# Kernel tuning notes

Measured on AMD Instinct MI355X. Metric: run time of the kernel, lower is better.

Reference implementation:

```python
import jax, jax.numpy as jnp
import numpy as np

N_NODES = 50000
N_EDGES = 800000
C_IN = 64
C_HID = 64


def setup_inputs() -> dict:
    key = jax.random.key(0)
    k1, k2, k3, k4, k5 = jax.random.split(key, 5)
    x = jax.random.normal(k1, (N_NODES, C_IN), dtype=jnp.float32)
    edge_index = jax.random.randint(k2, (2, N_EDGES), 0, N_NODES, dtype=jnp.int64)
    edge_attr = jax.random.uniform(k3, (N_EDGES, 1), dtype=jnp.float32)
    # SplineConv params: kernel weight (K=1 collapsed), root weight, bias
    W = jax.random.normal(k4, (C_IN, C_HID), dtype=jnp.float32) * (1.0 / np.sqrt(C_IN))
    root = jax.random.normal(k5, (C_IN, C_HID), dtype=jnp.float32) * (1.0 / np.sqrt(C_IN))
    bias = jnp.zeros((C_HID,), dtype=jnp.float32)
    return {"x": x, "edge_index": edge_index, "edge_attr": edge_attr,
            "W": W, "root": root, "bias": bias}


def reference(x, edge_index, edge_attr, W, root, bias):
    # SplineConv(dim=1, kernel_size=1): the B-spline basis weights sum to 1
    # over the single kernel, so message_j = x_j @ W exactly (edge_attr drops out).
    src = edge_index[0]  # source nodes j
    dst = edge_index[1]  # target nodes i
    n = x.shape[0]
    h = x @ W                                   # [N, H] transform once per node
    msg_sum = jax.ops.segment_sum(h[src], dst, num_segments=n)   # scatter-add [N, H]
    deg = jax.ops.segment_sum(jnp.ones_like(dst, dtype=h.dtype), dst, num_segments=n)
    agg = msg_sum / jnp.clip(deg, 1.0)[:, None]  # mean aggregation
    out = agg + x @ root + bias                  # root weight + bias
    return jax.nn.relu(out)
```

## Files before the change

### kernel.cpp

```cpp
#include <hip/hip_runtime.h>

#define N_NODES 50000
#define N_EDGES 800000
#define C 64
#define BUCKET_NODES 256
#define NBUCK 196
#define BUCKET_CAP 6144
#define BIN_CHUNK 4096
#define NBIN_BLOCKS 196
#define PREP_XBLOCKS 315
#define PB_BLOCKS (1 + PREP_XBLOCKS + NBIN_BLOCKS)
#define BIN0 (1 + PREP_XBLOCKS)
#define AGG_NODES 16
#define NAGG (N_NODES / AGG_NODES)
#define LDSTR 72

typedef __attribute__((ext_vector_type(8))) short bf16x8;
typedef __attribute__((ext_vector_type(4))) float f32x4;

__device__ inline unsigned short f2bf(float f) {
    union { float f; unsigned u; } v; v.f = f;
    unsigned r = v.u + 0x7FFF + ((v.u >> 16) & 1);
    return (unsigned short)(r >> 16);
}
__device__ inline float bf2f(unsigned short h) {
    union { unsigned u; float f; } v; v.u = (unsigned)h << 16;
    return v.f;
}

__global__ __launch_bounds__(256) void zero_cursor(int* __restrict__ c)
{
    c[threadIdx.x] = 0;
}

__global__ __launch_bounds__(256) void prep_bin(
    const float* __restrict__ x,
    const float* __restrict__ W,
    const float* __restrict__ R,
    const int*   __restrict__ ei,
    unsigned short* __restrict__ xbf,
    unsigned* __restrict__ xf8w,
    uint4* __restrict__ wpack,
    int* __restrict__ bucketCursor,
    int* __restrict__ bucketbuf)
{
    const int bid = blockIdx.x;

    if (bid == 0) {
        for (int s = threadIdx.x; s < 1024; s += 256) {
            const int f    = s >> 6;
            const int lane = s & 63;
            const int mat  = f >> 3, ks = (f >> 2) & 1, ct = f & 3;
            const float* src = mat ? R : W;
            const int kbase = ks * 32 + (lane >> 4) * 8;
            const int col   = ct * 16 + (lane & 15);
            unsigned wd[4];
            #pragma unroll
            for (int jj = 0; jj < 4; ++jj) {
                const unsigned lo16 = f2bf(src[(kbase + 2*jj    ) * C + col]);
                const unsigned hi16 = f2bf(src[(kbase + 2*jj + 1) * C + col]);
                wd[jj] = lo16 | (hi16 << 16);
            }
            uint4 o; o.x = wd[0]; o.y = wd[1]; o.z = wd[2]; o.w = wd[3];
            wpack[s] = o;
        }
        return;
    }

    if (bid < BIN0) {
        const int nthreads = PREP_XBLOCKS * 256;
        const int total4 = (N_NODES * C) / 4;
        for (int i = (bid - 1) * 256 + threadIdx.x; i < total4; i += nthreads) {
            const float4 v = ((const float4*)x)[i];
            ushort4 o;
            o.x = f2bf(v.x); o.y = f2bf(v.y); o.z = f2bf(v.z); o.w = f2bf(v.w);
            ((ushort4*)xbf)[i] = o;
            int w8 = __builtin_amdgcn_cvt_pk_fp8_f32(v.x, v.y, 0, false);
            w8     = __builtin_amdgcn_cvt_pk_fp8_f32(v.z, v.w, w8, true);
            xf8w[i] = (unsigned)w8;
        }
        return;
    }

    __shared__ int sdst[BIN_CHUNK];
    __shared__ int cnt[NBUCK], cnt2[NBUCK], gb[NBUCK];
    for (int i = threadIdx.x; i < NBUCK; i += 256) { cnt[i] = 0; cnt2[i] = 0; }
    __syncthreads();

    const int bb = bid - BIN0;
    const int e0 = bb * BIN_CHUNK;
    const int e1 = min(e0 + BIN_CHUNK, N_EDGES);
    const int ne = e1 - e0;

    for (int k = threadIdx.x; k < ne; k += 256) {
        const int d = ei[N_EDGES + e0 + k];
        sdst[k] = d;
        atomicAdd(&cnt[((unsigned)d) >> 8], 1);
    }
    __syncthreads();

    for (int i = threadIdx.x; i < NBUCK; i += 256)
        gb[i] = atomicAdd(&bucketCursor[i], cnt[i]);
    __syncthreads();

    for (int k = threadIdx.x; k < ne; k += 256) {
        const int src = ei[e0 + k];
        const int dst = sdst[k];
        const int bkt = ((unsigned)dst) >> 8;
        const int off = gb[bkt] + atomicAdd(&cnt2[bkt], 1);
        bucketbuf[bkt * BUCKET_CAP + off] = (src << 8) | (dst & 255);
    }
}

__global__ __launch_bounds__(512) void csr_place_scan(
    const int* __restrict__ bucketCursor,
    const int* __restrict__ bucketbuf,
    int* __restrict__ rowptr,
    int* __restrict__ ebuf)
{
    __shared__ int entries[BUCKET_CAP];
    __shared__ int lcur[BUCKET_NODES];
    __shared__ int wsum[4];
    __shared__ int boffS;

    const int b    = blockIdx.x;
    const int tid  = threadIdx.x;
    const int lane = tid & 63, w = tid >> 6;
    const int lo   = b * BUCKET_NODES;
    const int nn   = min(BUCKET_NODES, N_NODES - lo);
    const int cnt  = bucketCursor[b];

    if (w == 0) {
        const int base = lane * 4;
        int s0 = (base+0 < NBUCK) ? bucketCursor[base+0] : 0;
        int s1 = (base+1 < NBUCK) ? bucketCursor[base+1] : 0;
        int s2 = (base+2 < NBUCK) ? bucketCursor[base+2] : 0;
        int s3 = (base+3 < NBUCK) ? bucketCursor[base+3] : 0;
        const int tot = s0 + s1 + s2 + s3;
        int incl = tot;
        #pragma unroll
        for (int off = 1; off < 64; off <<= 1) {
            const int t = __shfl_up(incl, off);
            if (lane >= off) incl += t;
        }
        if (lane == (b >> 2)) {
            int v = incl - tot;
            if ((b & 3) > 0) v += s0;
            if ((b & 3) > 1) v += s1;
            if ((b & 3) > 2) v += s2;
            boffS = v;
        }
    }

    if (tid < BUCKET_NODES) lcur[tid] = 0;
    for (int k = tid; k < cnt; k += 512) entries[k] = bucketbuf[b * BUCKET_CAP + k];
    __syncthreads();

    for (int k = tid; k < cnt; k += 512)
        atomicAdd(&lcur[entries[k] & 255], 1);
    __syncthreads();

    int v = 0, incl = 0;
    if (tid < BUCKET_NODES) {
        v = (tid < nn) ? lcur[tid] : 0;
        incl = v;
        #pragma unroll
        for (int off = 1; off < 64; off <<= 1) {
            const int t = __shfl_up(incl, off);
            if (lane >= off) incl += t;
        }
        if (lane == 63) wsum[w] = incl;
    }
    __syncthreads();
    int excl = 0;
    if (tid < BUCKET_NODES) {
        int woff = boffS;
        for (int k2 = 0; k2 < 4; ++k2) if (k2 < w) woff += wsum[k2];
        excl = woff + incl - v;
    }
    __syncthreads();
    if (tid < nn) {
        rowptr[lo + tid] = excl;
        lcur[tid] = excl;
        if (lo + tid == N_NODES - 1) rowptr[N_NODES] = excl + v;
    }
    __syncthreads();

    for (int k = tid; k < cnt; k += 512) {
        const int p   = entries[k];
        const int pos = atomicAdd(&lcur[p & 255], 1);
        ebuf[pos] = p >> 8;
    }
}

__global__ __launch_bounds__(256) void agg_mfma(
    const int* __restrict__ rowptr,
    const int* __restrict__ ebuf,
    const unsigned short* __restrict__ xbf,
    const unsigned* __restrict__ xf8w,
    const uint4*  __restrict__ wpack,
    const float*  __restrict__ bias,
    float* __restrict__ out)
{
    __shared__ unsigned short aggs[AGG_NODES][LDSTR];

    const int lane = threadIdx.x & 63;
    const int w    = threadIdx.x >> 6;
    const int tileBase = (int)blockIdx.x * AGG_NODES;

    const int r = lane & 15;
    const int g = lane >> 4;

    #pragma unroll
    for (int i = 0; i < 4; ++i) {
        const int n   = tileBase + w * 4 + i;
        const int beg = rowptr[n];
        const int end = rowptr[n + 1];
        float a0 = 0.f, a1 = 0.f, a2 = 0.f, a3 = 0.f;
        for (int base = beg; base < end; base += 64) {
            const int m = min(64, end - base);
            const int sid = (base + lane < end) ? ebuf[base + lane] : 0;
            int j = 0;
            for (; j + 16 <= m; j += 16) {
                const int s0 = __shfl(sid, j + g);
                const int s1 = __shfl(sid, j + 4  + g);
                const int s2 = __shfl(sid, j + 8  + g);
                const int s3 = __shfl(sid, j + 12 + g);
                const unsigned u0 = xf8w[(size_t)s0 * 16 + r];
                const unsigned u1 = xf8w[(size_t)s1 * 16 + r];
                const unsigned u2 = xf8w[(size_t)s2 * 16 + r];
                const unsigned u3 = xf8w[(size_t)s3 * 16 + r];
                a0 += __builtin_amdgcn_cvt_f32_fp8((int)u0, 0) +
                      __builtin_amdgcn_cvt_f32_fp8((int)u1, 0) +
                      __builtin_amdgcn_cvt_f32_fp8((int)u2, 0) +
                      __builtin_amdgcn_cvt_f32_fp8((int)u3, 0);
                a1 += __builtin_amdgcn_cvt_f32_fp8((int)u0, 1) +
                      __builtin_amdgcn_cvt_f32_fp8((int)u1, 1) +
                      __builtin_amdgcn_cvt_f32_fp8((int)u2, 1) +
                      __builtin_amdgcn_cvt_f32_fp8((int)u3, 1);
                a2 += __builtin_amdgcn_cvt_f32_fp8((int)u0, 2) +
                      __builtin_amdgcn_cvt_f32_fp8((int)u1, 2) +
                      __builtin_amdgcn_cvt_f32_fp8((int)u2, 2) +
                      __builtin_amdgcn_cvt_f32_fp8((int)u3, 2);
                a3 += __builtin_amdgcn_cvt_f32_fp8((int)u0, 3) +
                      __builtin_amdgcn_cvt_f32_fp8((int)u1, 3) +
                      __builtin_amdgcn_cvt_f32_fp8((int)u2, 3) +
                      __builtin_amdgcn_cvt_f32_fp8((int)u3, 3);
            }
            for (; j < m; j += 4) {
                const int  e     = j + g;
                const bool valid = e < m;
                const int  s     = __shfl(sid, valid ? e : 0);
                const unsigned u = xf8w[(size_t)s * 16 + r];
                if (valid) {
                    a0 += __builtin_amdgcn_cvt_f32_fp8((int)u, 0);
                    a1 += __builtin_amdgcn_cvt_f32_fp8((int)u, 1);
                    a2 += __builtin_amdgcn_cvt_f32_fp8((int)u, 2);
                    a3 += __builtin_amdgcn_cvt_f32_fp8((int)u, 3);
                }
            }
        }
        #pragma unroll
        for (int off = 16; off <= 32; off <<= 1) {
            a0 += __shfl_xor(a0, off);
            a1 += __shfl_xor(a1, off);
            a2 += __shfl_xor(a2, off);
            a3 += __shfl_xor(a3, off);
        }
        if (g == 0) {
            const float inv = 1.0f / fmaxf((float)(end - beg), 1.0f);
            uint2 pv;
            pv.x = (unsigned)f2bf(a0 * inv) | ((unsigned)f2bf(a1 * inv) << 16);
            pv.y = (unsigned)f2bf(a2 * inv) | ((unsigned)f2bf(a3 * inv) << 16);
            *(uint2*)&aggs[w * 4 + i][r * 4] = pv;
        }
    }
    __syncthreads();

    const int q = lane >> 4;

    const bf16x8 bw0 = *(const bf16x8*)&wpack[(0*8 + 0*4 + w) * 64 + lane];
    const bf16x8 bw1 = *(const bf16x8*)&wpack[(0*8 + 1*4 + w) * 64 + lane];
    const bf16x8 br0 = *(const bf16x8*)&wpack[(1*8 + 0*4 + w) * 64 + lane];
    const bf16x8 br1 = *(const bf16x8*)&wpack[(1*8 + 1*4 + w) * 64 + lane];
    const float  bb  = bias[w * 16 + r];

    const unsigned short* rx = xbf + (size_t)(tileBase + r) * C;
    const bf16x8 a0 = *(const bf16x8*)&aggs[r][q * 8];
    const bf16x8 a1 = *(const bf16x8*)&aggs[r][32 + q * 8];
    const bf16x8 a2 = *(const bf16x8*)(rx + q * 8);
    const bf16x8 a3 = *(const bf16x8*)(rx + 32 + q * 8);

    f32x4 acc4 = {0.f, 0.f, 0.f, 0.f};
    acc4 = __builtin_amdgcn_mfma_f32_16x16x32_bf16(a0, bw0, acc4, 0, 0, 0);
    acc4 = __builtin_amdgcn_mfma_f32_16x16x32_bf16(a1, bw1, acc4, 0, 0, 0);
    acc4 = __builtin_amdgcn_mfma_f32_16x16x32_bf16(a2, br0, acc4, 0, 0, 0);
    acc4 = __builtin_amdgcn_mfma_f32_16x16x32_bf16(a3, br1, acc4, 0, 0, 0);

    #pragma unroll
    for (int i = 0; i < 4; ++i) {
        const int node = tileBase + q * 4 + i;
        out[(size_t)node * C + w * 16 + r] = fmaxf(acc4[i] + bb, 0.f);
    }
}

extern "C" void kernel_launch(void* const* d_in, const int* in_sizes, int n_in,
                              void* d_out, int out_size, void* d_ws, size_t ws_size,
                              hipStream_t stream)
{
    const float* x    = (const float*)d_in[0];
    const int*   ei   = (const int*)d_in[1];
    const float* W    = (const float*)d_in[3];
    const float* R    = (const float*)d_in[4];
    const float* bias = (const float*)d_in[5];

    char* wsb = (char*)d_ws;
    unsigned short* xbf = (unsigned short*)wsb;
    size_t off = (size_t)N_NODES * C * sizeof(unsigned short);
    unsigned* xf8w      = (unsigned*)(wsb + off); off += (size_t)N_NODES * 16 * sizeof(unsigned);
    uint4* wpack        = (uint4*)(wsb + off);  off += 1024 * sizeof(uint4);
    int*   bucketCursor = (int*)(wsb + off);    off += 256 * sizeof(int);
    int*   rowptr       = (int*)(wsb + off);    off += ((N_NODES + 8) & ~3) * sizeof(int);
    int*   ebuf         = (int*)(wsb + off);    off += (size_t)N_EDGES * sizeof(int);
    int*   bucketbuf    = (int*)(wsb + off);
    float* out          = (float*)d_out;

    zero_cursor   <<<1, 256, 0, stream>>>(bucketCursor);
    prep_bin      <<<PB_BLOCKS, 256, 0, stream>>>(x, W, R, ei, xbf, xf8w, wpack,
                                                  bucketCursor, bucketbuf);
    csr_place_scan<<<NBUCK, 512, 0, stream>>>(bucketCursor, bucketbuf, rowptr, ebuf);
    agg_mfma      <<<NAGG, 256, 0, stream>>>(rowptr, ebuf, xbf, xf8w, wpack, bias, out);
}
```

Before: 58.98 us.

## Split x conversion across prep_bin and CSR placement kernel to balance load

Moves half of the fp32-to-bf16/fp8 conversion of x out of prep_bin and into the CSR placement kernel, where extra blocks beyond the bucket blocks handle the second half. The placement kernel also goes from 512 to 1024 threads per block. The aim is to shorten the critical path of prep_bin and fill idle CUs during CSR placement, which only used 196 blocks. The cost is larger blocks that may lower occupancy, and the conversion work now competes with the scan for bandwidth.

```diff
diff --git a/kernel.cpp b/kernel.cpp
--- a/kernel.cpp
+++ b/kernel.cpp
@@ -11,6 +11,10 @@
 #define PREP_XBLOCKS 315
 #define PB_BLOCKS (1 + PREP_XBLOCKS + NBIN_BLOCKS)
 #define BIN0 (1 + PREP_XBLOCKS)
+#define TOTAL4 ((N_NODES * C) / 4)
+#define CONV_HALF 400000
+#define CSRCONV_BLOCKS 512
+#define CONVB_BLOCKS (CSRCONV_BLOCKS - NBUCK)
 #define AGG_NODES 16
 #define NAGG (N_NODES / AGG_NODES)
 #define LDSTR 72
@@ -26,6 +30,17 @@
 __device__ inline float bf2f(unsigned short h) {
     union { unsigned u; float f; } v; v.u = (unsigned)h << 16;
     return v.f;
+}
+
+__device__ inline void conv_one(const float4 v, unsigned short* xbf,
+                                unsigned* xf8w, int i)
+{
+    ushort4 o;
+    o.x = f2bf(v.x); o.y = f2bf(v.y); o.z = f2bf(v.z); o.w = f2bf(v.w);
+    ((ushort4*)xbf)[i] = o;
+    int w8 = __builtin_amdgcn_cvt_pk_fp8_f32(v.x, v.y, 0, false);
+    w8     = __builtin_amdgcn_cvt_pk_fp8_f32(v.z, v.w, w8, true);
+    xf8w[i] = (unsigned)w8;
 }
 
 __global__ __launch_bounds__(256) void zero_cursor(int* __restrict__ c)
@@ -69,16 +84,8 @@
 
     if (bid < BIN0) {
         const int nthreads = PREP_XBLOCKS * 256;
-        const int total4 = (N_NODES * C) / 4;
-        for (int i = (bid - 1) * 256 + threadIdx.x; i < total4; i += nthreads) {
-            const float4 v = ((const float4*)x)[i];
-            ushort4 o;
-            o.x = f2bf(v.x); o.y = f2bf(v.y); o.z = f2bf(v.z); o.w = f2bf(v.w);
-            ((ushort4*)xbf)[i] = o;
-            int w8 = __builtin_amdgcn_cvt_pk_fp8_f32(v.x, v.y, 0, false);
-            w8     = __builtin_amdgcn_cvt_pk_fp8_f32(v.z, v.w, w8, true);
-            xf8w[i] = (unsigned)w8;
-        }
+        for (int i = (bid - 1) * 256 + threadIdx.x; i < CONV_HALF; i += nthreads)
+            conv_one(((const float4*)x)[i], xbf, xf8w, i);
         return;
     }
 
@@ -112,19 +119,31 @@
     }
 }
 
-__global__ __launch_bounds__(512) void csr_place_scan(
+__global__ __launch_bounds__(1024) void csr_conv(
+    const float* __restrict__ x,
     const int* __restrict__ bucketCursor,
     const int* __restrict__ bucketbuf,
     int* __restrict__ rowptr,
-    int* __restrict__ ebuf)
-{
+    int* __restrict__ ebuf,
+    unsigned short* __restrict__ xbf,
+    unsigned* __restrict__ xf8w)
+{
+    const int bid = blockIdx.x;
+    const int tid = threadIdx.x;
+
+    if (bid >= NBUCK) {
+        const int nthreads = CONVB_BLOCKS * 1024;
+        for (int i = CONV_HALF + (bid - NBUCK) * 1024 + tid; i < TOTAL4; i += nthreads)
+            conv_one(((const float4*)x)[i], xbf, xf8w, i);
+        return;
+    }
+
     __shared__ int entries[BUCKET_CAP];
     __shared__ int lcur[BUCKET_NODES];
     __shared__ int wsum[4];
     __shared__ int boffS;
 
-    const int b    = blockIdx.x;
-    const int tid  = threadIdx.x;
+    const int b    = bid;
     const int lane = tid & 63, w = tid >> 6;
     const int lo   = b * BUCKET_NODES;
     const int nn   = min(BUCKET_NODES, N_NODES - lo);
@@ -153,10 +172,10 @@
     }
 
     if (tid < BUCKET_NODES) lcur[tid] = 0;
-    for (int k = tid; k < cnt; k += 512) entries[k] = bucketbuf[b * BUCKET_CAP + k];
-    __syncthreads();
-
-    for (int k = tid; k < cnt; k += 512)
+    for (int k = tid; k < cnt; k += 1024) entries[k] = bucketbuf[b * BUCKET_CAP + k];
+    __syncthreads();
+
+    for (int k = tid; k < cnt; k += 1024)
         atomicAdd(&lcur[entries[k] & 255], 1);
     __syncthreads();
 
@@ -186,7 +205,7 @@
     }
     __syncthreads();
 
-    for (int k = tid; k < cnt; k += 512) {
+    for (int k = tid; k < cnt; k += 1024) {
         const int p   = entries[k];
         const int pos = atomicAdd(&lcur[p & 255], 1);
         ebuf[pos] = p >> 8;
@@ -325,9 +344,10 @@
     int*   bucketbuf    = (int*)(wsb + off);
     float* out          = (float*)d_out;
 
-    zero_cursor   <<<1, 256, 0, stream>>>(bucketCursor);
-    prep_bin      <<<PB_BLOCKS, 256, 0, stream>>>(x, W, R, ei, xbf, xf8w, wpack,
-                                                  bucketCursor, bucketbuf);
-    csr_place_scan<<<NBUCK, 512, 0, stream>>>(bucketCursor, bucketbuf, rowptr, ebuf);
-    agg_mfma      <<<NAGG, 256, 0, stream>>>(rowptr, ebuf, xbf, xf8w, wpack, bias, out);
-}
+    zero_cursor<<<1, 256, 0, stream>>>(bucketCursor);
+    prep_bin   <<<PB_BLOCKS, 256, 0, stream>>>(x, W, R, ei, xbf, xf8w, wpack,
+                                               bucketCursor, bucketbuf);
+    csr_conv   <<<CSRCONV_BLOCKS, 1024, 0, stream>>>(x, bucketCursor, bucketbuf,
+                                                     rowptr, ebuf, xbf, xf8w);
+    agg_mfma   <<<NAGG, 256, 0, stream>>>(rowptr, ebuf, xbf, xf8w, wpack, bias, out);
+}
```

Measured after the change: 59.71 us. No clear change (+1.2%).
